# Performance work log

Hardware: AMD Instinct MI355X
Metric: run time of the kernel (lower is better)

Reference implementation:

```python
import jax, jax.numpy as jnp
import numpy as np

B, S, N, D = 2048, 8, 32, 64


def setup_inputs() -> dict:
    key = jax.random.key(0)
    ks = jax.random.split(key, 13)
    s1 = 1.0 / np.sqrt(2 * D + 6)
    s2 = 1.0 / np.sqrt(D)
    s3 = 1.0 / np.sqrt(D // 2)
    return {
        "celestial_tensor": jax.random.normal(ks[0], (B, S, N, D), jnp.float32),
        "theta": jax.random.normal(ks[1], (B, N), jnp.float32),
        "phi": jax.random.normal(ks[2], (B, N), jnp.float32),
        "velocity": jax.random.normal(ks[3], (B, N), jnp.float32),
        "radius": jax.random.uniform(ks[4], (B, N), jnp.float32),
        "longitude": jax.random.normal(ks[5], (B, N), jnp.float32),
        "W1": jax.random.uniform(ks[6], (2 * D + 6, D), jnp.float32, -s1, s1),
        "b1": jax.random.uniform(ks[7], (D,), jnp.float32, -s1, s1),
        "W2": jax.random.uniform(ks[8], (D, D // 2), jnp.float32, -s2, s2),
        "b2": jax.random.uniform(ks[9], (D // 2,), jnp.float32, -s2, s2),
        "W3": jax.random.uniform(ks[10], (D // 2, 1), jnp.float32, -s3, s3),
        "b3": jax.random.uniform(ks[11], (1,), jnp.float32, -s3, s3),
        "phase_weights": jnp.ones((6,), jnp.float32),
    }


def _circ(a, b):
    # circular difference wrapped to (-pi, pi]
    d = a - b
    return jnp.arctan2(jnp.sin(d), jnp.cos(d))


def reference(celestial_tensor, theta, phi, velocity, radius, longitude,
              W1, b1, W2, b2, W3, b3, phase_weights):
    Bb, _, Nn, _ = celestial_tensor.shape
    feats = celestial_tensor[:, -1]  # [B, N, D] last timestep
    ii, jj = np.triu_indices(Nn, 1)  # static upper-tri pair indices, P pairs
    fi = feats[:, ii]  # [B, P, D]
    fj = feats[:, jj]
    td = _circ(theta[:, ii], theta[:, jj])
    pd = _circ(phi[:, ii], phi[:, jj])
    vd = velocity[:, ii] - velocity[:, jj]
    rr = radius[:, ii] / (radius[:, jj] + 1e-8)
    ld = _circ(longitude[:, ii], longitude[:, jj])
    pr = jnp.cos(td) * jnp.cos(pd)  # phase_relationship
    scal = jnp.stack([td, pd, vd, rr, ld, pr], axis=-1)  # [B, P, 6]
    x = jnp.concatenate([fi, fj, scal], axis=-1)  # [B, P, 2D+6]
    h = jax.nn.gelu(x @ W1 + b1, approximate=False)
    h = jax.nn.gelu(h @ W2 + b2, approximate=False)
    edge = jax.nn.sigmoid((h @ W3 + b3)[..., 0])  # [B, P]
    pf = jnp.stack([jnp.abs(td), jnp.abs(pd), jnp.abs(vd),
                    jnp.abs(rr - 1.0), jnp.abs(ld), jnp.abs(pr)], axis=-1)
    gate = jax.nn.sigmoid(jnp.sum(pf * phase_weights, axis=-1))
    fe = edge * gate  # [B, P]
    adj = jnp.zeros((Bb, Nn, Nn), dtype=fe.dtype)
    adj = adj.at[:, ii, jj].set(fe).at[:, jj, ii].set(fe)
    return adj
```

## Files before the change

### kernel.cpp

```cpp
#include <hip/hip_runtime.h>
#include <hip/hip_bf16.h>
#include <math.h>

#define SS 8
#define NN 32
#define DD 64
#define NP 496
#define LDA 68

typedef short v8s __attribute__((ext_vector_type(8)));
typedef float v4f __attribute__((ext_vector_type(4)));
typedef float f2  __attribute__((ext_vector_type(2)));

union FragU { uint4 u; v8s s; };
union Q2    { float4 q; f2 h[2]; };

static __device__ __forceinline__ f2 f2m(float a, float b) { f2 r; r.x = a; r.y = b; return r; }
static __device__ __forceinline__ f2 splat2(float s) { f2 r; r.x = s; r.y = s; return r; }
static __device__ __forceinline__ f2 pk_fma(f2 a, f2 b, f2 c) {
#if __has_builtin(__builtin_elementwise_fma)
    return __builtin_elementwise_fma(a, b, c);
#else
    return f2m(fmaf(a.x, b.x, c.x), fmaf(a.y, b.y, c.y));
#endif
}

__device__ __forceinline__ float wrap_pi(float d) {
    return fmaf(-6.28318530717958647692f, rintf(d * 0.15915494309189533577f), d);
}
__device__ __forceinline__ float sigmoid_(float x) {
    return __builtin_amdgcn_rcpf(1.0f + __expf(-x));
}
__device__ __forceinline__ f2 gelu2(f2 x) {
#if __has_builtin(__builtin_elementwise_max)
    f2 ax = __builtin_elementwise_max(x, -x);
#else
    f2 ax = f2m(fabsf(x.x), fabsf(x.y));
#endif
    f2 az = ax * splat2(0.70710678118654752440f);
    f2 d = pk_fma(splat2(0.078108f), az, splat2(0.000972f));
    d = pk_fma(d, az, splat2(0.230389f));
    d = pk_fma(d, az, splat2(0.278393f));
    d = pk_fma(d, az, splat2(1.0f));
    f2 t = f2m(__builtin_amdgcn_rcpf(d.x), __builtin_amdgcn_rcpf(d.y));
    f2 t2 = t * t;
    f2 a = ax * splat2(0.5f);
    f2 base = pk_fma(x, splat2(0.5f), a);
    f2 u = a * t2;
    return pk_fma(-u, t2, base);
}
__device__ __forceinline__ unsigned int pack_bf16_rne(float x0, float x1) {
    union { __hip_bfloat162 h2; unsigned int u; } cv;
    float2 f; f.x = x0; f.y = x1;
    cv.h2 = __float22bfloat162_rn(f);
    return cv.u;
}
__device__ __forceinline__ unsigned int res_pack(unsigned int hw, float x0, float x1) {
    const float f0 = __uint_as_float(hw << 16);
    const float f1 = __uint_as_float(hw & 0xFFFF0000u);
    return pack_bf16_rne(x0 - f0, x1 - f1);
}
__device__ __forceinline__ float row_reduce16(float x) {
    int v;
    v = __builtin_amdgcn_update_dpp(0, __float_as_int(x), 0x128, 0xf, 0xf, false);
    x += __int_as_float(v);
    v = __builtin_amdgcn_update_dpp(0, __float_as_int(x), 0x124, 0xf, 0xf, false);
    x += __int_as_float(v);
    v = __builtin_amdgcn_update_dpp(0, __float_as_int(x), 0x122, 0xf, 0xf, false);
    x += __int_as_float(v);
    v = __builtin_amdgcn_update_dpp(0, __float_as_int(x), 0x121, 0xf, 0xf, false);
    x += __int_as_float(v);
    return x;
}
__device__ __forceinline__ uint4 build_w2_frag(const float* __restrict__ W2,
                                               int kb, int col) {
    uint4 pk;
    pk.x = pack_bf16_rne(W2[(kb + 0) * 32 + col], W2[(kb + 1) * 32 + col]);
    pk.y = pack_bf16_rne(W2[(kb + 2) * 32 + col], W2[(kb + 3) * 32 + col]);
    pk.z = pack_bf16_rne(W2[(kb + 4) * 32 + col], W2[(kb + 5) * 32 + col]);
    pk.w = pack_bf16_rne(W2[(kb + 6) * 32 + col], W2[(kb + 7) * 32 + col]);
    return pk;
}

__global__ __launch_bounds__(256, 2) void edge_kernel(
    const float* __restrict__ cel,
    const float* __restrict__ theta,
    const float* __restrict__ phi,
    const float* __restrict__ vel,
    const float* __restrict__ rad,
    const float* __restrict__ lon,
    const float* __restrict__ W1,
    const float* __restrict__ b1,
    const float* __restrict__ W2,
    const float* __restrict__ b2,
    const float* __restrict__ W3,
    const float* __restrict__ b3,
    const float* __restrict__ pw,
    float* __restrict__ out)
{
    __shared__ __align__(16) float sAi[NN * LDA];
    __shared__ __align__(16) float sBj[NN * LDA];
    __shared__ float sAdj[1024];
    __shared__ __align__(16) float sScal[NP * 8];
    __shared__ unsigned char sI[NP], sJ[NP];

    const int b = blockIdx.x;
    const int t = threadIdx.x;
    const int ml = t & 15;
    const int ql = (t >> 4) & 3;
    const int wv = t >> 6;
    const int kA = ql * 8;

    FragU f00, f01, f10, f11;
    f00.u = build_w2_frag(W2, 0 * 32 + kA, 0 * 16 + ml);
    f01.u = build_w2_frag(W2, 1 * 32 + kA, 0 * 16 + ml);
    f10.u = build_w2_frag(W2, 0 * 32 + kA, 1 * 16 + ml);
    f11.u = build_w2_frag(W2, 1 * 32 + kA, 1 * 16 + ml);
    const float b2v0 = b2[ml], b2v1 = b2[16 + ml];
    const float w3v0 = W3[ml], w3v1 = W3[16 + ml];
    const float b3s  = b3[0];

    if (t < 31) {
        int off = t * 31 - (t * (t - 1)) / 2;
        for (int j = t + 1; j < 32; ++j) {
            sI[off] = (unsigned char)t;
            sJ[off] = (unsigned char)j;
            ++off;
        }
    }
    for (int idx = t; idx < 1024; idx += 256) sAdj[idx] = 0.0f;
    __syncthreads();

    for (int p = t; p < NP; p += 256) {
        const int i = sI[p], j = sJ[p];
        const float td = wrap_pi(theta[b * NN + i] - theta[b * NN + j]);
        const float pd = wrap_pi(phi[b * NN + i] - phi[b * NN + j]);
        const float vd = vel[b * NN + i] - vel[b * NN + j];
        const float rr = rad[b * NN + i] * __builtin_amdgcn_rcpf(rad[b * NN + j] + 1e-8f);
        const float ld = wrap_pi(lon[b * NN + i] - lon[b * NN + j]);
        const float pr = __cosf(td) * __cosf(pd);
        const float pf = fabsf(td) * pw[0] + fabsf(pd) * pw[1]
                       + fabsf(vd) * pw[2] + fabsf(rr - 1.0f) * pw[3]
                       + fabsf(ld) * pw[4] + fabsf(pr) * pw[5];
        const int sw = (p >> 2) & 1;
        float4* c0 = (float4*)&sScal[p * 8 + (sw << 2)];
        float4* c1 = (float4*)&sScal[p * 8 + ((sw ^ 1) << 2)];
        *c0 = float4{td, pd, vd, rr};
        *c1 = float4{ld, pr, sigmoid_(pf), 0.0f};
    }

    {
        const int w4 = __builtin_amdgcn_readfirstlane(t >> 6);
        const int tg = w4 >> 1;
        const int mt = w4 & 1;
        const float* fbase = cel + ((size_t)b * SS + (SS - 1)) * (NN * DD);
        const float* Arow = fbase + (mt * 16 + ml) * 64;
        const float4 e0 = *(const float4*)(Arow + kA);
        const float4 e1 = *(const float4*)(Arow + kA + 4);
        const float4 e2 = *(const float4*)(Arow + 32 + kA);
        const float4 e3 = *(const float4*)(Arow + 36 + kA);
        FragU Ah0, Al0, Ah1, Al1;
        Ah0.u.x = pack_bf16_rne(e0.x, e0.y);
        Ah0.u.y = pack_bf16_rne(e0.z, e0.w);
        Ah0.u.z = pack_bf16_rne(e1.x, e1.y);
        Ah0.u.w = pack_bf16_rne(e1.z, e1.w);
        Al0.u.x = res_pack(Ah0.u.x, e0.x, e0.y);
        Al0.u.y = res_pack(Ah0.u.y, e0.z, e0.w);
        Al0.u.z = res_pack(Ah0.u.z, e1.x, e1.y);
        Al0.u.w = res_pack(Ah0.u.w, e1.z, e1.w);
        Ah1.u.x = pack_bf16_rne(e2.x, e2.y);
        Ah1.u.y = pack_bf16_rne(e2.z, e2.w);
        Ah1.u.z = pack_bf16_rne(e3.x, e3.y);
        Ah1.u.w = pack_bf16_rne(e3.z, e3.w);
        Al1.u.x = res_pack(Ah1.u.x, e2.x, e2.y);
        Al1.u.y = res_pack(Ah1.u.y, e2.z, e2.w);
        Al1.u.z = res_pack(Ah1.u.z, e3.x, e3.y);
        Al1.u.w = res_pack(Ah1.u.w, e3.z, e3.w);

        const float* WB = W1 + (tg * 64) * 64;
        float* dstS = tg ? sBj : sAi;
        #pragma clang loop unroll(disable)
        for (int nt = 0; nt < 4; ++nt) {
            const int colb = nt * 16 + ml;
            const float* B0p = WB + kA * 64 + colb;
            const float* B1p = WB + (32 + kA) * 64 + colb;
            FragU B0, B1;
            B0.u.x = pack_bf16_rne(B0p[0],   B0p[64]);
            B0.u.y = pack_bf16_rne(B0p[128], B0p[192]);
            B0.u.z = pack_bf16_rne(B0p[256], B0p[320]);
            B0.u.w = pack_bf16_rne(B0p[384], B0p[448]);
            B1.u.x = pack_bf16_rne(B1p[0],   B1p[64]);
            B1.u.y = pack_bf16_rne(B1p[128], B1p[192]);
            B1.u.z = pack_bf16_rne(B1p[256], B1p[320]);
            B1.u.w = pack_bf16_rne(B1p[384], B1p[448]);
            const float cinit = tg ? 0.0f : b1[colb];
            v4f acc = {cinit, cinit, cinit, cinit};
            acc = __builtin_amdgcn_mfma_f32_16x16x32_bf16(Ah0.s, B0.s, acc, 0, 0, 0);
            acc = __builtin_amdgcn_mfma_f32_16x16x32_bf16(Al0.s, B0.s, acc, 0, 0, 0);
            acc = __builtin_amdgcn_mfma_f32_16x16x32_bf16(Ah1.s, B1.s, acc, 0, 0, 0);
            acc = __builtin_amdgcn_mfma_f32_16x16x32_bf16(Al1.s, B1.s, acc, 0, 0, 0);
            dstS[(mt * 16 + ql * 4 + 0) * LDA + colb] = acc[0];
            dstS[(mt * 16 + ql * 4 + 1) * LDA + colb] = acc[1];
            dstS[(mt * 16 + ql * 4 + 2) * LDA + colb] = acc[2];
            dstS[(mt * 16 + ql * 4 + 3) * LDA + colb] = acc[3];
        }
    }
    __syncthreads();

    const float* W1s = W1 + 128 * 64;
    f2 w1f[6][8];
    #pragma unroll
    for (int s = 0; s < 6; ++s) {
        Q2 u0, u1, u2, u3;
        u0.q = *(const float4*)&W1s[s * 64 + kA];
        u1.q = *(const float4*)&W1s[s * 64 + kA + 4];
        u2.q = *(const float4*)&W1s[s * 64 + 32 + kA];
        u3.q = *(const float4*)&W1s[s * 64 + 36 + kA];
        w1f[s][0] = u0.h[0]; w1f[s][1] = u0.h[1];
        w1f[s][2] = u1.h[0]; w1f[s][3] = u1.h[1];
        w1f[s][4] = u2.h[0]; w1f[s][5] = u2.h[1];
        w1f[s][6] = u3.h[0]; w1f[s][7] = u3.h[1];
    }

    #pragma clang loop unroll(disable)
    for (int r = 0; r < 8; ++r) {
        const int mtl = r * 4 + wv;
        if (mtl >= 31) break;
        const int p = mtl * 16 + ml;
        const int i = sI[p], j = sJ[p];
        const int sw = (p >> 2) & 1;
        Q2 S0, S1;
        S0.q = *(const float4*)&sScal[p * 8 + (sw << 2)];
        S1.q = *(const float4*)&sScal[p * 8 + ((sw ^ 1) << 2)];
        const float sc[6] = {S0.q.x, S0.q.y, S0.q.z, S0.q.w, S1.q.x, S1.q.y};
        const float* Ar = &sAi[i * LDA];
        const float* Br = &sBj[j * LDA];

        FragU fa0, fa1;
        {
            Q2 P0, P1, Q0, Q1;
            P0.q = *(const float4*)(Ar + kA);
            P1.q = *(const float4*)(Ar + kA + 4);
            Q0.q = *(const float4*)(Br + kA);
            Q1.q = *(const float4*)(Br + kA + 4);
            f2 v[4] = {P0.h[0] + Q0.h[0], P0.h[1] + Q0.h[1],
                       P1.h[0] + Q1.h[0], P1.h[1] + Q1.h[1]};
            #pragma unroll
            for (int s = 0; s < 6; ++s) {
                const f2 scs = splat2(sc[s]);
                #pragma unroll
                for (int c = 0; c < 4; ++c)
                    v[c] = pk_fma(scs, w1f[s][c], v[c]);
            }
            #pragma unroll
            for (int c = 0; c < 4; ++c) v[c] = gelu2(v[c]);
            fa0.u.x = pack_bf16_rne(v[0].x, v[0].y);
            fa0.u.y = pack_bf16_rne(v[1].x, v[1].y);
            fa0.u.z = pack_bf16_rne(v[2].x, v[2].y);
            fa0.u.w = pack_bf16_rne(v[3].x, v[3].y);
        }
        {
            Q2 P2, P3, Q2v, Q3;
            P2.q  = *(const float4*)(Ar + 32 + kA);
            P3.q  = *(const float4*)(Ar + 36 + kA);
            Q2v.q = *(const float4*)(Br + 32 + kA);
            Q3.q  = *(const float4*)(Br + 36 + kA);
            f2 y[4] = {P2.h[0] + Q2v.h[0], P2.h[1] + Q2v.h[1],
                       P3.h[0] + Q3.h[0],  P3.h[1] + Q3.h[1]};
            #pragma unroll
            for (int s = 0; s < 6; ++s) {
                const f2 scs = splat2(sc[s]);
                #pragma unroll
                for (int c = 0; c < 4; ++c)
                    y[c] = pk_fma(scs, w1f[s][4 + c], y[c]);
            }
            #pragma unroll
            for (int c = 0; c < 4; ++c) y[c] = gelu2(y[c]);
            fa1.u.x = pack_bf16_rne(y[0].x, y[0].y);
            fa1.u.y = pack_bf16_rne(y[1].x, y[1].y);
            fa1.u.z = pack_bf16_rne(y[2].x, y[2].y);
            fa1.u.w = pack_bf16_rne(y[3].x, y[3].y);
        }

        v4f acc0 = {b2v0, b2v0, b2v0, b2v0};
        v4f acc1 = {b2v1, b2v1, b2v1, b2v1};
        acc0 = __builtin_amdgcn_mfma_f32_16x16x32_bf16(fa0.s, f00.s, acc0, 0, 0, 0);
        acc0 = __builtin_amdgcn_mfma_f32_16x16x32_bf16(fa1.s, f01.s, acc0, 0, 0, 0);
        acc1 = __builtin_amdgcn_mfma_f32_16x16x32_bf16(fa0.s, f10.s, acc1, 0, 0, 0);
        acc1 = __builtin_amdgcn_mfma_f32_16x16x32_bf16(fa1.s, f11.s, acc1, 0, 0, 0);

        float cres[4];
        #pragma unroll
        for (int rr = 0; rr < 4; ++rr) {
            const f2 g = gelu2(f2m(acc0[rr], acc1[rr]));
            cres[rr] = row_reduce16(fmaf(g.y, w3v1, g.x * w3v0));
        }
        const int rsel = ml & 3;
        const float cs = (rsel & 2) ? ((rsel & 1) ? cres[3] : cres[2])
                                    : ((rsel & 1) ? cres[1] : cres[0]);
        const int pe = mtl * 16 + ql * 4 + rsel;
        const int swe = (pe >> 2) & 1;
        const float gate = sScal[pe * 8 + ((swe ^ 1) << 2) + 2];
        const float fe = sigmoid_(cs + b3s) * gate;
        if (ml < 4) {
            const int pi = sI[pe], pj = sJ[pe];
            sAdj[pi * 32 + pj] = fe;
            sAdj[pj * 32 + pi] = fe;
        }
    }
    __syncthreads();

    float* dst = out + (size_t)b * 1024;
    for (int idx = t; idx < 1024; idx += 256) dst[idx] = sAdj[idx];
}

extern "C" void kernel_launch(void* const* d_in, const int* in_sizes, int n_in,
                              void* d_out, int out_size, void* d_ws, size_t ws_size,
                              hipStream_t stream) {
    const float* cel   = (const float*)d_in[0];
    const float* theta = (const float*)d_in[1];
    const float* phi   = (const float*)d_in[2];
    const float* vel   = (const float*)d_in[3];
    const float* rad   = (const float*)d_in[4];
    const float* lon   = (const float*)d_in[5];
    const float* W1    = (const float*)d_in[6];
    const float* b1    = (const float*)d_in[7];
    const float* W2    = (const float*)d_in[8];
    const float* b2    = (const float*)d_in[9];
    const float* W3    = (const float*)d_in[10];
    const float* b3    = (const float*)d_in[11];
    const float* pw    = (const float*)d_in[12];
    float* out = (float*)d_out;

    const int B = in_sizes[1] / NN;
    edge_kernel<<<B, 256, 0, stream>>>(cel, theta, phi, vel, rad, lon,
                                       W1, b1, W2, b2, W3, b3, pw, out);
}
```

Baseline: 238.8 us.

## Switch layer-1 pair stage to packed fp16 math with fp16 MFMA

Stores the per-node layer-1 projections in shared memory as fp16 instead of fp32. The per-pair scalar FMAs and the first GELU now run as 8-wide packed half-precision vectors, and layer 2 uses fp16 MFMA with fp16 W2 fragments in place of bf16. This is meant to halve LDS traffic and double packed ALU throughput in the hot pair loop, and it drops the bf16 packing step. In exchange it loses precision in the GELU and in the accumulation of pre-activations, and it needs a clamp on the radius ratio to avoid fp16 overflow.

```diff
diff --git a/kernel.cpp b/kernel.cpp
--- a/kernel.cpp
+++ b/kernel.cpp
@@ -6,11 +6,12 @@
 #define NN 32
 #define DD 64
 #define NP 496
-#define LDA 68
+#define LDAH 72
 
 typedef short v8s __attribute__((ext_vector_type(8)));
 typedef float v4f __attribute__((ext_vector_type(4)));
 typedef float f2  __attribute__((ext_vector_type(2)));
+typedef _Float16 h8v __attribute__((ext_vector_type(8)));
 
 union FragU { uint4 u; v8s s; };
 union Q2    { float4 q; f2 h[2]; };
@@ -23,6 +24,15 @@
 #else
     return f2m(fmaf(a.x, b.x, c.x), fmaf(a.y, b.y, c.y));
 #endif
+}
+static __device__ __forceinline__ h8v splat8h(float s) {
+    const _Float16 h = (_Float16)s;
+    h8v r = {h, h, h, h, h, h, h, h};
+    return r;
+}
+static __device__ __forceinline__ h8v splat8hh(_Float16 h) {
+    h8v r = {h, h, h, h, h, h, h, h};
+    return r;
 }
 
 __device__ __forceinline__ float wrap_pi(float d) {
@@ -49,6 +59,27 @@
     f2 u = a * t2;
     return pk_fma(-u, t2, base);
 }
+__device__ __forceinline__ h8v gelu8h(h8v x) {
+    h8v ax = __builtin_elementwise_max(x, -x);
+    h8v az = ax * splat8h(0.70710678118654752440f);
+    h8v d = __builtin_elementwise_fma(splat8h(0.078108f), az, splat8h(0.000972f));
+    d = __builtin_elementwise_fma(d, az, splat8h(0.230389f));
+    d = __builtin_elementwise_fma(d, az, splat8h(0.278393f));
+    d = __builtin_elementwise_fma(d, az, splat8h(1.0f));
+    h8v t;
+    #pragma unroll
+    for (int k = 0; k < 8; ++k)
+#if __has_builtin(__builtin_amdgcn_rcph)
+        t[k] = __builtin_amdgcn_rcph(d[k]);
+#else
+        t[k] = (_Float16)__builtin_amdgcn_rcpf((float)d[k]);
+#endif
+    h8v t2 = t * t;
+    h8v a = ax * splat8h(0.5f);
+    h8v base = __builtin_elementwise_fma(x, splat8h(0.5f), a);
+    h8v u = a * t2;
+    return __builtin_elementwise_fma(-u, t2, base);
+}
 __device__ __forceinline__ unsigned int pack_bf16_rne(float x0, float x1) {
     union { __hip_bfloat162 h2; unsigned int u; } cv;
     float2 f; f.x = x0; f.y = x1;
@@ -72,14 +103,12 @@
     x += __int_as_float(v);
     return x;
 }
-__device__ __forceinline__ uint4 build_w2_frag(const float* __restrict__ W2,
-                                               int kb, int col) {
-    uint4 pk;
-    pk.x = pack_bf16_rne(W2[(kb + 0) * 32 + col], W2[(kb + 1) * 32 + col]);
-    pk.y = pack_bf16_rne(W2[(kb + 2) * 32 + col], W2[(kb + 3) * 32 + col]);
-    pk.z = pack_bf16_rne(W2[(kb + 4) * 32 + col], W2[(kb + 5) * 32 + col]);
-    pk.w = pack_bf16_rne(W2[(kb + 6) * 32 + col], W2[(kb + 7) * 32 + col]);
-    return pk;
+__device__ __forceinline__ h8v build_w2_fragh(const float* __restrict__ W2,
+                                              int kb, int col) {
+    h8v r;
+    #pragma unroll
+    for (int k = 0; k < 8; ++k) r[k] = (_Float16)W2[(kb + k) * 32 + col];
+    return r;
 }
 
 __global__ __launch_bounds__(256, 2) void edge_kernel(
@@ -98,8 +127,8 @@
     const float* __restrict__ pw,
     float* __restrict__ out)
 {
-    __shared__ __align__(16) float sAi[NN * LDA];
-    __shared__ __align__(16) float sBj[NN * LDA];
+    __shared__ __align__(16) _Float16 sAiH[NN * LDAH];
+    __shared__ __align__(16) _Float16 sBjH[NN * LDAH];
     __shared__ float sAdj[1024];
     __shared__ __align__(16) float sScal[NP * 8];
     __shared__ unsigned char sI[NP], sJ[NP];
@@ -111,11 +140,10 @@
     const int wv = t >> 6;
     const int kA = ql * 8;
 
-    FragU f00, f01, f10, f11;
-    f00.u = build_w2_frag(W2, 0 * 32 + kA, 0 * 16 + ml);
-    f01.u = build_w2_frag(W2, 1 * 32 + kA, 0 * 16 + ml);
-    f10.u = build_w2_frag(W2, 0 * 32 + kA, 1 * 16 + ml);
-    f11.u = build_w2_frag(W2, 1 * 32 + kA, 1 * 16 + ml);
+    h8v f00h = build_w2_fragh(W2, 0 * 32 + kA, 0 * 16 + ml);
+    h8v f01h = build_w2_fragh(W2, 1 * 32 + kA, 0 * 16 + ml);
+    h8v f10h = build_w2_fragh(W2, 0 * 32 + kA, 1 * 16 + ml);
+    h8v f11h = build_w2_fragh(W2, 1 * 32 + kA, 1 * 16 + ml);
     const float b2v0 = b2[ml], b2v1 = b2[16 + ml];
     const float w3v0 = W3[ml], w3v1 = W3[16 + ml];
     const float b3s  = b3[0];
@@ -178,7 +206,7 @@
         Al1.u.w = res_pack(Ah1.u.w, e3.z, e3.w);
 
         const float* WB = W1 + (tg * 64) * 64;
-        float* dstS = tg ? sBj : sAi;
+        _Float16* dstS = tg ? sBjH : sAiH;
         #pragma clang loop unroll(disable)
         for (int nt = 0; nt < 4; ++nt) {
             const int colb = nt * 16 + ml;
@@ -199,27 +227,26 @@
             acc = __builtin_amdgcn_mfma_f32_16x16x32_bf16(Al0.s, B0.s, acc, 0, 0, 0);
             acc = __builtin_amdgcn_mfma_f32_16x16x32_bf16(Ah1.s, B1.s, acc, 0, 0, 0);
             acc = __builtin_amdgcn_mfma_f32_16x16x32_bf16(Al1.s, B1.s, acc, 0, 0, 0);
-            dstS[(mt * 16 + ql * 4 + 0) * LDA + colb] = acc[0];
-            dstS[(mt * 16 + ql * 4 + 1) * LDA + colb] = acc[1];
-            dstS[(mt * 16 + ql * 4 + 2) * LDA + colb] = acc[2];
-            dstS[(mt * 16 + ql * 4 + 3) * LDA + colb] = acc[3];
+            dstS[(mt * 16 + ql * 4 + 0) * LDAH + colb] = (_Float16)acc[0];
+            dstS[(mt * 16 + ql * 4 + 1) * LDAH + colb] = (_Float16)acc[1];
+            dstS[(mt * 16 + ql * 4 + 2) * LDAH + colb] = (_Float16)acc[2];
+            dstS[(mt * 16 + ql * 4 + 3) * LDAH + colb] = (_Float16)acc[3];
         }
     }
     __syncthreads();
 
     const float* W1s = W1 + 128 * 64;
-    f2 w1f[6][8];
+    h8v w1fh[6][2];
     #pragma unroll
     for (int s = 0; s < 6; ++s) {
-        Q2 u0, u1, u2, u3;
-        u0.q = *(const float4*)&W1s[s * 64 + kA];
-        u1.q = *(const float4*)&W1s[s * 64 + kA + 4];
-        u2.q = *(const float4*)&W1s[s * 64 + 32 + kA];
-        u3.q = *(const float4*)&W1s[s * 64 + 36 + kA];
-        w1f[s][0] = u0.h[0]; w1f[s][1] = u0.h[1];
-        w1f[s][2] = u1.h[0]; w1f[s][3] = u1.h[1];
-        w1f[s][4] = u2.h[0]; w1f[s][5] = u2.h[1];
-        w1f[s][6] = u3.h[0]; w1f[s][7] = u3.h[1];
+        const float4 u0 = *(const float4*)&W1s[s * 64 + kA];
+        const float4 u1 = *(const float4*)&W1s[s * 64 + kA + 4];
+        const float4 u2 = *(const float4*)&W1s[s * 64 + 32 + kA];
+        const float4 u3 = *(const float4*)&W1s[s * 64 + 36 + kA];
+        w1fh[s][0] = h8v{(_Float16)u0.x, (_Float16)u0.y, (_Float16)u0.z, (_Float16)u0.w,
+                         (_Float16)u1.x, (_Float16)u1.y, (_Float16)u1.z, (_Float16)u1.w};
+        w1fh[s][1] = h8v{(_Float16)u2.x, (_Float16)u2.y, (_Float16)u2.z, (_Float16)u2.w,
+                         (_Float16)u3.x, (_Float16)u3.y, (_Float16)u3.z, (_Float16)u3.w};
     }
 
     #pragma clang loop unroll(disable)
@@ -232,68 +259,46 @@
         Q2 S0, S1;
         S0.q = *(const float4*)&sScal[p * 8 + (sw << 2)];
         S1.q = *(const float4*)&sScal[p * 8 + ((sw ^ 1) << 2)];
-        const float sc[6] = {S0.q.x, S0.q.y, S0.q.z, S0.q.w, S1.q.x, S1.q.y};
-        const float* Ar = &sAi[i * LDA];
-        const float* Br = &sBj[j * LDA];
-
-        FragU fa0, fa1;
+        const _Float16 sch[6] = {
+            (_Float16)S0.q.x, (_Float16)S0.q.y, (_Float16)S0.q.z,
+            (_Float16)fminf(S0.q.w, 30000.0f),
+            (_Float16)S1.q.x, (_Float16)S1.q.y};
+        const _Float16* ArH = &sAiH[i * LDAH];
+        const _Float16* BrH = &sBjH[j * LDAH];
+
+        h8v v0;
         {
-            Q2 P0, P1, Q0, Q1;
-            P0.q = *(const float4*)(Ar + kA);
-            P1.q = *(const float4*)(Ar + kA + 4);
-            Q0.q = *(const float4*)(Br + kA);
-            Q1.q = *(const float4*)(Br + kA + 4);
-            f2 v[4] = {P0.h[0] + Q0.h[0], P0.h[1] + Q0.h[1],
-                       P1.h[0] + Q1.h[0], P1.h[1] + Q1.h[1]};
+            const h8v P = *(const h8v*)(ArH + kA);
+            const h8v Q = *(const h8v*)(BrH + kA);
+            h8v v = P + Q;
             #pragma unroll
-            for (int s = 0; s < 6; ++s) {
-                const f2 scs = splat2(sc[s]);
-                #pragma unroll
-                for (int c = 0; c < 4; ++c)
-                    v[c] = pk_fma(scs, w1f[s][c], v[c]);
-            }
+            for (int s = 0; s < 6; ++s)
+                v = __builtin_elementwise_fma(splat8hh(sch[s]), w1fh[s][0], v);
+            v0 = gelu8h(v);
+        }
+        h8v v1;
+        {
+            const h8v P = *(const h8v*)(ArH + 32 + kA);
+            const h8v Q = *(const h8v*)(BrH + 32 + kA);
+            h8v y = P + Q;
             #pragma unroll
-            for (int c = 0; c < 4; ++c) v[c] = gelu2(v[c]);
-            fa0.u.x = pack_bf16_rne(v[0].x, v[0].y);
-            fa0.u.y = pack_bf16_rne(v[1].x, v[1].y);
-            fa0.u.z = pack_bf16_rne(v[2].x, v[2].y);
-            fa0.u.w = pack_bf16_rne(v[3].x, v[3].y);
-        }
-        {
-            Q2 P2, P3, Q2v, Q3;
-            P2.q  = *(const float4*)(Ar + 32 + kA);
-            P3.q  = *(const float4*)(Ar + 36 + kA);
-            Q2v.q = *(const float4*)(Br + 32 + kA);
-            Q3.q  = *(const float4*)(Br + 36 + kA);
-            f2 y[4] = {P2.h[0] + Q2v.h[0], P2.h[1] + Q2v.h[1],
-                       P3.h[0] + Q3.h[0],  P3.h[1] + Q3.h[1]};
-            #pragma unroll
-            for (int s = 0; s < 6; ++s) {
-                const f2 scs = splat2(sc[s]);
-                #pragma unroll
-                for (int c = 0; c < 4; ++c)
-                    y[c] = pk_fma(scs, w1f[s][4 + c], y[c]);
-            }
-            #pragma unroll
-            for (int c = 0; c < 4; ++c) y[c] = gelu2(y[c]);
-            fa1.u.x = pack_bf16_rne(y[0].x, y[0].y);
-            fa1.u.y = pack_bf16_rne(y[1].x, y[1].y);
-            fa1.u.z = pack_bf16_rne(y[2].x, y[2].y);
-            fa1.u.w = pack_bf16_rne(y[3].x, y[3].y);
+            for (int s = 0; s < 6; ++s)
+                y = __builtin_elementwise_fma(splat8hh(sch[s]), w1fh[s][1], y);
+            v1 = gelu8h(y);
         }
 
         v4f acc0 = {b2v0, b2v0, b2v0, b2v0};
         v4f acc1 = {b2v1, b2v1, b2v1, b2v1};
-        acc0 = __builtin_amdgcn_mfma_f32_16x16x32_bf16(fa0.s, f00.s, acc0, 0, 0, 0);
-        acc0 = __builtin_amdgcn_mfma_f32_16x16x32_bf16(fa1.s, f01.s, acc0, 0, 0, 0);
-        acc1 = __builtin_amdgcn_mfma_f32_16x16x32_bf16(fa0.s, f10.s, acc1, 0, 0, 0);
-        acc1 = __builtin_amdgcn_mfma_f32_16x16x32_bf16(fa1.s, f11.s, acc1, 0, 0, 0);
+        acc0 = __builtin_amdgcn_mfma_f32_16x16x32_f16(v0, f00h, acc0, 0, 0, 0);
+        acc0 = __builtin_amdgcn_mfma_f32_16x16x32_f16(v1, f01h, acc0, 0, 0, 0);
+        acc1 = __builtin_amdgcn_mfma_f32_16x16x32_f16(v0, f10h, acc1, 0, 0, 0);
+        acc1 = __builtin_amdgcn_mfma_f32_16x16x32_f16(v1, f11h, acc1, 0, 0, 0);
 
         float cres[4];
         #pragma unroll
-        for (int rr = 0; rr < 4; ++rr) {
-            const f2 g = gelu2(f2m(acc0[rr], acc1[rr]));
-            cres[rr] = row_reduce16(fmaf(g.y, w3v1, g.x * w3v0));
+        for (int rr2 = 0; rr2 < 4; ++rr2) {
+            const f2 g = gelu2(f2m(acc0[rr2], acc1[rr2]));
+            cres[rr2] = row_reduce16(fmaf(g.y, w3v1, g.x * w3v0));
         }
         const int rsel = ml & 3;
         const float cs = (rsel & 2) ? ((rsel & 1) ? cres[3] : cres[2])
```

New measurement: 237.5 us. No clear change (-0.5%).
